# Kernel tuning notes

Measured on AMD Instinct MI355X. Metric: run time of the kernel, lower is better.

The kernel has to match this reference:

```python
import jax, jax.numpy as jnp
import numpy as np

N_NODES = 100000
N_EDGES = 3200000
N_FEAT = 128
N_GRAPHS = 256
N_CLASSES = 10


def setup_inputs() -> dict:
    key = jax.random.key(0)
    ks = jax.random.split(key, 10)
    x = jax.random.normal(ks[0], (N_NODES, N_FEAT), dtype=jnp.float32)
    edge_index = jax.random.randint(ks[1], (2, N_EDGES), 0, N_NODES, dtype=jnp.int64)
    batch = jnp.sort(jax.random.randint(ks[2], (N_NODES,), 0, N_GRAPHS, dtype=jnp.int64))
    # GCNConv weights (glorot-ish scaling) and biases
    W1 = jax.random.normal(ks[3], (N_FEAT, 16), dtype=jnp.float32) / np.sqrt(N_FEAT)
    b1 = jnp.zeros((16,), dtype=jnp.float32)
    W2 = jax.random.normal(ks[4], (16, 32), dtype=jnp.float32) / np.sqrt(16.0)
    b2 = jnp.zeros((32,), dtype=jnp.float32)
    Wfc = jax.random.normal(ks[5], (32, N_CLASSES), dtype=jnp.float32) / np.sqrt(32.0)
    bfc = jnp.zeros((N_CLASSES,), dtype=jnp.float32)
    return {"x": x, "edge_index": edge_index, "batch": batch,
            "W1": W1, "b1": b1, "W2": W2, "b2": b2, "Wfc": Wfc, "bfc": bfc}


def reference(x, edge_index, batch, W1, b1, W2, b2, Wfc, bfc):
    N = x.shape[0]
    # --- GCN normalization with self-loops (PyG GCNConv default) ---
    loop = jnp.arange(N, dtype=edge_index.dtype)
    src = jnp.concatenate([edge_index[0], loop])  # [E+N]
    dst = jnp.concatenate([edge_index[1], loop])  # [E+N]
    ones = jnp.ones_like(src, dtype=x.dtype)
    deg = jax.ops.segment_sum(ones, dst, num_segments=N)  # in-degree incl self-loop
    dinv = jax.lax.rsqrt(deg)  # deg >= 1 thanks to self-loops
    norm = dinv[src] * dinv[dst]  # [E+N]

    def gcn_conv(h, W, b):
        h = h @ W                               # [N, out] linear first (small out dim)
        msg = h[src] * norm[:, None]            # gather + edge-wise scale
        agg = jax.ops.segment_sum(msg, dst, num_segments=N)  # scatter-add
        return agg + b

    h = jax.nn.relu(gcn_conv(x, W1, b1))
    h = jax.nn.relu(gcn_conv(h, W2, b2))

    # --- global mean pool over graphs ---
    g_sum = jax.ops.segment_sum(h, batch, num_segments=N_GRAPHS)  # [G, 32]
    g_cnt = jax.ops.segment_sum(jnp.ones((N,), dtype=h.dtype), batch, num_segments=N_GRAPHS)
    pooled = g_sum / jnp.maximum(g_cnt, 1.0)[:, None]

    return pooled @ Wfc + bfc  # [G, num_classes]
```

## Files before the change

kernel.cpp:

```cpp
#include <hip/hip_runtime.h>
#include <hip/hip_fp16.h>

#define NF   128
#define C1   16
#define C2   32
#define NCLS 10
#define BSH  8
#define BN   256
#define MAXB 512
#define S    9216
#define TILE 4096
#define EPT  (TILE/256)
#define CAP  12288


__global__ __launch_bounds__(256) void k_bin(const int* __restrict__ ei,
                                             int* __restrict__ packed,
                                             int* __restrict__ offmat,
                                             int E, int nbuck) {
    __shared__ int hist[MAXB];
    __shared__ int off0[MAXB];
    __shared__ int cur[MAXB];
    int tid = threadIdx.x;
    long long t0 = (long long)blockIdx.x * TILE;

    for (int i = tid; i < MAXB; i += 256) hist[i] = 0;
    __syncthreads();

    int dstv[EPT], srcv[EPT];
#pragma unroll
    for (int u = 0; u < EPT; ++u) {
        long long e = t0 + tid + u * 256;
        int d = -1, s = 0;
        if (e < E) { d = ei[E + e]; s = ei[e]; }
        dstv[u] = d; srcv[u] = s;
        if (d >= 0) atomicAdd(&hist[d >> BSH], 1);
    }
    __syncthreads();
    if (tid < 64) {
        int carry = 0;
        for (int c = 0; c < MAXB / 64; ++c) {
            int idx = c * 64 + tid;
            int v = hist[idx];
            int orig = v;
            for (int off = 1; off < 64; off <<= 1) {
                int t = __shfl_up(v, off);
                if (tid >= off) v += t;
            }
            int ex = v - orig + carry;
            off0[idx] = ex;
            cur[idx] = ex;
            carry += __shfl(v, 63);
        }
    }
    __syncthreads();
    int* orow = offmat + (size_t)blockIdx.x * (nbuck + 1);
    for (int b = tid; b <= nbuck; b += 256) orow[b] = off0[b];
#pragma unroll
    for (int u = 0; u < EPT; ++u) {
        int d = dstv[u];
        if (d >= 0) {
            int b = d >> BSH;
            int slot = atomicAdd(&cur[b], 1);
            packed[t0 + slot] = srcv[u] | ((d & (BN - 1)) << 17);
        }
    }
}


__global__ __launch_bounds__(1024) void k_csr(const int* __restrict__ packed,
                                              const int* __restrict__ offmat,
                                              int* __restrict__ csr,
                                              int* __restrict__ rowptr,
                                              int* __restrict__ deg,
                                              float* __restrict__ dinv,
                                              int N, int nbuck, int nblkA) {
    __shared__ int stage[CAP];
    __shared__ int startA[1024];
    __shared__ int spsA[1024];
    __shared__ int o1A[1024];
    __shared__ int hcnt[BN];
    __shared__ int sh[BN];
    __shared__ int cur[BN];
    int tid = threadIdx.x;
    int b = blockIdx.x;
    size_t base = (size_t)b * S;

    int len = 0, o1 = 0;
    if (tid < nblkA) {
        const int* orow = offmat + (size_t)tid * (nbuck + 1) + b;
        o1 = orow[0];
        len = orow[1] - o1;
    }
    o1A[tid] = o1;
    spsA[tid] = len;
    if (tid < BN) hcnt[tid] = 0;
    __syncthreads();
    for (int off = 1; off < 1024; off <<= 1) {
        int t = (tid >= off) ? spsA[tid - off] : 0;
        __syncthreads();
        spsA[tid] += t;
        __syncthreads();
    }
    int m = spsA[1023];
    startA[tid] = spsA[tid] - len;
    __syncthreads();
    if (m > CAP) m = CAP;

    for (int i = tid; i < m; i += 1024) {
        int lo = 0, hi = 1023;
        while (lo < hi) {
            int mid = (lo + hi + 1) >> 1;
            if (startA[mid] <= i) lo = mid; else hi = mid - 1;
        }
        int p = packed[(size_t)lo * TILE + o1A[lo] + (i - startA[lo])];
        stage[i] = p;
        atomicAdd(&hcnt[p >> 17], 1);
    }
    __syncthreads();
    int v = 0;
    if (tid < BN) { v = hcnt[tid]; sh[tid] = v; }
    __syncthreads();
    for (int off = 1; off < BN; off <<= 1) {
        int t = (tid < BN && tid >= off) ? sh[tid - off] : 0;
        __syncthreads();
        if (tid < BN) sh[tid] += t;
        __syncthreads();
    }
    if (tid < BN) {
        int ex = sh[tid] - v;
        cur[tid] = ex;
        int n = (b << BSH) + tid;
        if (n < N) {
            rowptr[n] = (int)base + ex;
            deg[n] = v;
            dinv[n] = rsqrtf((float)v + 1.0f);
        }
    }
    __syncthreads();
    for (int i = tid; i < m; i += 1024) {
        int p = stage[i];
        int slot = atomicAdd(&cur[p >> 17], 1);
        csr[base + slot] = p & 0x1FFFF;
    }
}


__global__ __launch_bounds__(256) void k_lin1(const float* __restrict__ x,
                                              const float* __restrict__ W1,
                                              const float* __restrict__ dinv,
                                              __half* __restrict__ y1h, int N) {
    __shared__ float ws[NF * C1];
    __shared__ float xs[16 * 132];
    int tid = threadIdx.x;
    for (int t = tid; t < NF * C1; t += 256) ws[t] = W1[t];
    int n0 = blockIdx.x * 16;
    const float4* x4 = (const float4*)x;
    for (int t = tid; t < 16 * 32; t += 256) {
        int r = t >> 5, c = t & 31;
        int n = n0 + r;
        float4 v = (n < N) ? x4[(size_t)n * 32 + c] : make_float4(0.f, 0.f, 0.f, 0.f);
        float* d = &xs[r * 132 + c * 4];
        d[0] = v.x; d[1] = v.y; d[2] = v.z; d[3] = v.w;
    }
    __syncthreads();
    int r = tid >> 4, j = tid & 15;
    float acc = 0.0f;
#pragma unroll 4
    for (int k = 0; k < NF; ++k) acc += xs[r * 132 + k] * ws[k * C1 + j];
    int n = n0 + r;
    if (n < N) y1h[(size_t)n * C1 + j] = __float2half_rn(acc * dinv[n]);
}


template <int MODE>
__global__ __launch_bounds__(256) void k_gather_h(const int* __restrict__ rowptr,
                                                  const int* __restrict__ deg,
                                                  const int* __restrict__ csr,
                                                  const float* __restrict__ dinv,
                                                  const float* __restrict__ bias,
                                                  const __half2* __restrict__ yh,
                                                  void* __restrict__ outp, int N) {
    int tid = threadIdx.x;
    int j = tid & 7;
    int n = blockIdx.x * 32 + (tid >> 3);
    if (n >= N) return;
    int k0 = rowptr[n];
    int k1 = k0 + deg[n];
    float2 self = __half22float2(yh[(size_t)n * 8 + j]);
    float a0 = self.x, a1 = self.y;
    float e0 = 0.f, e1 = 0.f, f0 = 0.f, f1 = 0.f, g0 = 0.f, g1 = 0.f;
    int k = k0;
    for (; k + 3 < k1; k += 4) {
        int s0 = csr[k], s1 = csr[k + 1], s2 = csr[k + 2], s3 = csr[k + 3];
        float2 v0 = __half22float2(yh[(size_t)s0 * 8 + j]);
        float2 v1 = __half22float2(yh[(size_t)s1 * 8 + j]);
        float2 v2 = __half22float2(yh[(size_t)s2 * 8 + j]);
        float2 v3 = __half22float2(yh[(size_t)s3 * 8 + j]);
        a0 += v0.x; a1 += v0.y; e0 += v1.x; e1 += v1.y;
        f0 += v2.x; f1 += v2.y; g0 += v3.x; g1 += v3.y;
    }
    for (; k < k1; ++k) {
        float2 v = __half22float2(yh[(size_t)csr[k] * 8 + j]);
        a0 += v.x; a1 += v.y;
    }
    float dn = dinv[n];
    float rx = dn * ((a0 + e0) + (f0 + g0));
    float ry = dn * ((a1 + e1) + (f1 + g1));
    if (MODE == 0) {
        ((float2*)outp)[(size_t)n * 8 + j] = make_float2(rx, ry);
    } else {
        float2 bb = ((const float2*)bias)[j];
        float u0 = fmaxf(rx + bb.x, 0.0f) * dn;
        float u1 = fmaxf(ry + bb.y, 0.0f) * dn;
        ((__half2*)outp)[(size_t)n * 8 + j] = __floats2half2_rn(u0, u1);
    }
}


__global__ __launch_bounds__(256) void k_pool_fc(const float* __restrict__ z,
                                                 const float* __restrict__ W2,
                                                 const float* __restrict__ b2,
                                                 const int* __restrict__ batch,
                                                 const float* __restrict__ Wfc,
                                                 const float* __restrict__ bfc,
                                                 float* __restrict__ out, int N, int G) {
    __shared__ float W2s[C1 * C2];
    int tid = threadIdx.x;
    for (int t = tid; t < C1 * C2; t += 256) W2s[t] = W2[t];

    int g = blockIdx.x;
    int lo = 0, hi = N;
    while (lo < hi) { int m = (lo + hi) >> 1; if (batch[m] < g) lo = m + 1; else hi = m; }
    int start = lo;
    lo = start; hi = N;
    while (lo < hi) { int m = (lo + hi) >> 1; if (batch[m] < g + 1) lo = m + 1; else hi = m; }
    int end = lo;
    __syncthreads();

    int i = tid & 31, r = tid >> 5;
    float bi = b2[i];
    float acc = 0.0f;
    for (int n = start + r; n < end; n += 8) {
        const float* zr = &z[(size_t)n * C1];
        float h = bi;
#pragma unroll
        for (int j = 0; j < C1; ++j) h += zr[j] * W2s[j * C2 + i];
        acc += fmaxf(h, 0.0f);
    }

    __shared__ float red[256];
    red[tid] = acc;
    __syncthreads();
    for (int s = 4; s >= 1; s >>= 1) {
        if (r < s) red[tid] += red[tid + s * 32];
        __syncthreads();
    }
    __shared__ float pooled[C2];
    if (tid < C2) {
        float cnt = (float)(end - start);
        pooled[tid] = red[tid] / fmaxf(cnt, 1.0f);
    }
    __syncthreads();
    if (tid < NCLS) {
        float a = bfc[tid];
#pragma unroll
        for (int j = 0; j < C2; ++j) a += pooled[j] * Wfc[j * NCLS + tid];
        out[g * NCLS + tid] = a;
    }
}

extern "C" void kernel_launch(void* const* d_in, const int* in_sizes, int n_in,
                              void* d_out, int out_size, void* d_ws, size_t ws_size,
                              hipStream_t stream) {
    const float* x    = (const float*)d_in[0];
    const int*   ei   = (const int*)d_in[1];
    const int*   batch= (const int*)d_in[2];
    const float* W1   = (const float*)d_in[3];
    const float* b1   = (const float*)d_in[4];
    const float* W2   = (const float*)d_in[5];
    const float* b2   = (const float*)d_in[6];
    const float* Wfc  = (const float*)d_in[7];
    const float* bfc  = (const float*)d_in[8];
    float* out = (float*)d_out;

    const int N = in_sizes[0] / NF;
    const int E = in_sizes[1] / 2;
    const int G = out_size / NCLS;
    const int nbuck = (N + BN - 1) >> BSH;
    const int nblkA = (E + TILE - 1) / TILE;

    char* p = (char*)d_ws;
    auto alloc = [&](size_t bytes) { char* q = p; p += (bytes + 63) & ~(size_t)63; return q; };
    int*     rowptr  = (int*)    alloc((size_t)N * 4);
    int*     deg     = (int*)    alloc((size_t)N * 4);
    float*   dinv    = (float*)  alloc((size_t)N * 4);
    int*     packed  = (int*)    alloc((size_t)nblkA * TILE * 4);
    int*     offmat  = (int*)    alloc((size_t)nblkA * (nbuck + 1) * 4);
    int*     csr     = (int*)    alloc((size_t)nbuck * S * 4);
    __half*  y1h     = (__half*) alloc((size_t)N * C1 * 2);
    __half*  uh      = (__half*) alloc((size_t)N * C1 * 2);
    float*   z       = (float*)  alloc((size_t)N * C1 * 4);

    const int B = 256;

    k_bin<<<nblkA, B, 0, stream>>>(ei, packed, offmat, E, nbuck);
    k_csr<<<nbuck, 1024, 0, stream>>>(packed, offmat, csr, rowptr, deg, dinv,
                                      N, nbuck, nblkA);

    k_lin1<<<(N + 15) / 16, B, 0, stream>>>(x, W1, dinv, y1h, N);
    k_gather_h<1><<<(N + 31) / 32, B, 0, stream>>>(rowptr, deg, csr, dinv, b1,
                                                   (const __half2*)y1h, uh, N);

    k_gather_h<0><<<(N + 31) / 32, B, 0, stream>>>(rowptr, deg, csr, dinv, b1,
                                                   (const __half2*)uh, z, N);

    k_pool_fc<<<G, B, 0, stream>>>(z, W2, b2, batch, Wfc, bfc, out, N, G);
}
```

Measured before the change: 170.1 us.

## Fuse edge binning with first linear layer and widen gather loads

Edge binning and the x@W1 product now run as one launch with blocks split by index, using a union of their shared-memory layouts. Because dinv is not known yet, the dinv scaling of y1 moves into the tail of the CSR build kernel, which rescales each bucket's rows in place. This removes a launch and lets the dense matmul overlap the binning. The gather kernel now has each thread load 8 bytes (four halves) instead of 4, so 4 threads cover a node and a block handles 64 nodes. The cost is an extra read-modify-write pass over y1h inside k_csr and fewer independent accumulators per thread.

```diff
diff --git a/kernel.cpp b/kernel.cpp
--- a/kernel.cpp
+++ b/kernel.cpp
@@ -14,56 +14,82 @@
 #define CAP  12288
 
 
-__global__ __launch_bounds__(256) void k_bin(const int* __restrict__ ei,
+struct BinSh { int hist[MAXB]; int off0[MAXB]; int cur[MAXB]; };
+struct LinSh { float ws[NF * C1]; float xs[16 * 132]; };
+union FatSh { BinSh b; LinSh l; };
+
+__global__ __launch_bounds__(256) void k_fat(const int* __restrict__ ei,
                                              int* __restrict__ packed,
                                              int* __restrict__ offmat,
-                                             int E, int nbuck) {
-    __shared__ int hist[MAXB];
-    __shared__ int off0[MAXB];
-    __shared__ int cur[MAXB];
+                                             const float* __restrict__ x,
+                                             const float* __restrict__ W1,
+                                             __half* __restrict__ y1h,
+                                             int E, int nbuck, int nblkA, int N) {
+    __shared__ FatSh sm;
     int tid = threadIdx.x;
-    long long t0 = (long long)blockIdx.x * TILE;
-
-    for (int i = tid; i < MAXB; i += 256) hist[i] = 0;
-    __syncthreads();
-
-    int dstv[EPT], srcv[EPT];
+
+    if (blockIdx.x < nblkA) {
+        long long t0 = (long long)blockIdx.x * TILE;
+        for (int i = tid; i < MAXB; i += 256) sm.b.hist[i] = 0;
+        __syncthreads();
+
+        int dstv[EPT], srcv[EPT];
 #pragma unroll
-    for (int u = 0; u < EPT; ++u) {
-        long long e = t0 + tid + u * 256;
-        int d = -1, s = 0;
-        if (e < E) { d = ei[E + e]; s = ei[e]; }
-        dstv[u] = d; srcv[u] = s;
-        if (d >= 0) atomicAdd(&hist[d >> BSH], 1);
-    }
-    __syncthreads();
-    if (tid < 64) {
-        int carry = 0;
-        for (int c = 0; c < MAXB / 64; ++c) {
-            int idx = c * 64 + tid;
-            int v = hist[idx];
-            int orig = v;
-            for (int off = 1; off < 64; off <<= 1) {
-                int t = __shfl_up(v, off);
-                if (tid >= off) v += t;
+        for (int u = 0; u < EPT; ++u) {
+            long long e = t0 + tid + u * 256;
+            int d = -1, s = 0;
+            if (e < E) { d = ei[E + e]; s = ei[e]; }
+            dstv[u] = d; srcv[u] = s;
+            if (d >= 0) atomicAdd(&sm.b.hist[d >> BSH], 1);
+        }
+        __syncthreads();
+        if (tid < 64) {
+            int carry = 0;
+            for (int c = 0; c < MAXB / 64; ++c) {
+                int idx = c * 64 + tid;
+                int v = sm.b.hist[idx];
+                int orig = v;
+                for (int off = 1; off < 64; off <<= 1) {
+                    int t = __shfl_up(v, off);
+                    if (tid >= off) v += t;
+                }
+                int ex = v - orig + carry;
+                sm.b.off0[idx] = ex;
+                sm.b.cur[idx] = ex;
+                carry += __shfl(v, 63);
             }
-            int ex = v - orig + carry;
-            off0[idx] = ex;
-            cur[idx] = ex;
-            carry += __shfl(v, 63);
-        }
-    }
-    __syncthreads();
-    int* orow = offmat + (size_t)blockIdx.x * (nbuck + 1);
-    for (int b = tid; b <= nbuck; b += 256) orow[b] = off0[b];
+        }
+        __syncthreads();
+        int* orow = offmat + (size_t)blockIdx.x * (nbuck + 1);
+        for (int b = tid; b <= nbuck; b += 256) orow[b] = sm.b.off0[b];
 #pragma unroll
-    for (int u = 0; u < EPT; ++u) {
-        int d = dstv[u];
-        if (d >= 0) {
-            int b = d >> BSH;
-            int slot = atomicAdd(&cur[b], 1);
-            packed[t0 + slot] = srcv[u] | ((d & (BN - 1)) << 17);
-        }
+        for (int u = 0; u < EPT; ++u) {
+            int d = dstv[u];
+            if (d >= 0) {
+                int b = d >> BSH;
+                int slot = atomicAdd(&sm.b.cur[b], 1);
+                packed[t0 + slot] = srcv[u] | ((d & (BN - 1)) << 17);
+            }
+        }
+    } else {
+        int bid = blockIdx.x - nblkA;
+        for (int t = tid; t < NF * C1; t += 256) sm.l.ws[t] = W1[t];
+        int n0 = bid * 16;
+        const float4* x4 = (const float4*)x;
+        for (int t = tid; t < 16 * 32; t += 256) {
+            int r = t >> 5, c = t & 31;
+            int n = n0 + r;
+            float4 v = (n < N) ? x4[(size_t)n * 32 + c] : make_float4(0.f, 0.f, 0.f, 0.f);
+            float* d = &sm.l.xs[r * 132 + c * 4];
+            d[0] = v.x; d[1] = v.y; d[2] = v.z; d[3] = v.w;
+        }
+        __syncthreads();
+        int r = tid >> 4, j = tid & 15;
+        float acc = 0.0f;
+#pragma unroll 4
+        for (int k = 0; k < NF; ++k) acc += sm.l.xs[r * 132 + k] * sm.l.ws[k * C1 + j];
+        int n = n0 + r;
+        if (n < N) y1h[(size_t)n * C1 + j] = __float2half_rn(acc);
     }
 }
 
@@ -74,6 +100,7 @@
                                               int* __restrict__ rowptr,
                                               int* __restrict__ deg,
                                               float* __restrict__ dinv,
+                                              __half* __restrict__ y1h,
                                               int N, int nbuck, int nblkA) {
     __shared__ int stage[CAP];
     __shared__ int startA[1024];
@@ -82,6 +109,7 @@
     __shared__ int hcnt[BN];
     __shared__ int sh[BN];
     __shared__ int cur[BN];
+    __shared__ float fdinv[BN];
     int tid = threadIdx.x;
     int b = blockIdx.x;
     size_t base = (size_t)b * S;
@@ -130,11 +158,13 @@
     if (tid < BN) {
         int ex = sh[tid] - v;
         cur[tid] = ex;
+        float dv = rsqrtf((float)v + 1.0f);
+        fdinv[tid] = dv;
         int n = (b << BSH) + tid;
         if (n < N) {
             rowptr[n] = (int)base + ex;
             deg[n] = v;
-            dinv[n] = rsqrtf((float)v + 1.0f);
+            dinv[n] = dv;
         }
     }
     __syncthreads();
@@ -143,33 +173,17 @@
         int slot = atomicAdd(&cur[p >> 17], 1);
         csr[base + slot] = p & 0x1FFFF;
     }
-}
-
-
-__global__ __launch_bounds__(256) void k_lin1(const float* __restrict__ x,
-                                              const float* __restrict__ W1,
-                                              const float* __restrict__ dinv,
-                                              __half* __restrict__ y1h, int N) {
-    __shared__ float ws[NF * C1];
-    __shared__ float xs[16 * 132];
-    int tid = threadIdx.x;
-    for (int t = tid; t < NF * C1; t += 256) ws[t] = W1[t];
-    int n0 = blockIdx.x * 16;
-    const float4* x4 = (const float4*)x;
-    for (int t = tid; t < 16 * 32; t += 256) {
-        int r = t >> 5, c = t & 31;
-        int n = n0 + r;
-        float4 v = (n < N) ? x4[(size_t)n * 32 + c] : make_float4(0.f, 0.f, 0.f, 0.f);
-        float* d = &xs[r * 132 + c * 4];
-        d[0] = v.x; d[1] = v.y; d[2] = v.z; d[3] = v.w;
-    }
-    __syncthreads();
-    int r = tid >> 4, j = tid & 15;
-    float acc = 0.0f;
-#pragma unroll 4
-    for (int k = 0; k < NF; ++k) acc += xs[r * 132 + k] * ws[k * C1 + j];
-    int n = n0 + r;
-    if (n < N) y1h[(size_t)n * C1 + j] = __float2half_rn(acc * dinv[n]);
+    int n0 = b << BSH;
+    int lim = min(BN, N - n0);
+    if (lim > 0) {
+        __half2* yrow = (__half2*)y1h + (size_t)n0 * 8;
+        int tot = lim * 8;
+        for (int i = tid; i < tot; i += 1024) {
+            float dv = fdinv[i >> 3];
+            float2 f = __half22float2(yrow[i]);
+            yrow[i] = __floats2half2_rn(f.x * dv, f.y * dv);
+        }
+    }
 }
 
 
@@ -179,41 +193,52 @@
                                                   const int* __restrict__ csr,
                                                   const float* __restrict__ dinv,
                                                   const float* __restrict__ bias,
-                                                  const __half2* __restrict__ yh,
+                                                  const uint2* __restrict__ yh,
                                                   void* __restrict__ outp, int N) {
     int tid = threadIdx.x;
-    int j = tid & 7;
-    int n = blockIdx.x * 32 + (tid >> 3);
+    int j = tid & 3;
+    int n = blockIdx.x * 64 + (tid >> 2);
     if (n >= N) return;
     int k0 = rowptr[n];
     int k1 = k0 + deg[n];
-    float2 self = __half22float2(yh[(size_t)n * 8 + j]);
-    float a0 = self.x, a1 = self.y;
-    float e0 = 0.f, e1 = 0.f, f0 = 0.f, f1 = 0.f, g0 = 0.f, g1 = 0.f;
+    union U { uint2 u; __half2 h[2]; };
+    U su; su.u = yh[(size_t)n * 4 + j];
+    float2 sl = __half22float2(su.h[0]), shh = __half22float2(su.h[1]);
+    float a0 = sl.x, a1 = sl.y, a2 = shh.x, a3 = shh.y;
+    float b0 = 0.f, b1v = 0.f, b2 = 0.f, b3 = 0.f;
     int k = k0;
     for (; k + 3 < k1; k += 4) {
         int s0 = csr[k], s1 = csr[k + 1], s2 = csr[k + 2], s3 = csr[k + 3];
-        float2 v0 = __half22float2(yh[(size_t)s0 * 8 + j]);
-        float2 v1 = __half22float2(yh[(size_t)s1 * 8 + j]);
-        float2 v2 = __half22float2(yh[(size_t)s2 * 8 + j]);
-        float2 v3 = __half22float2(yh[(size_t)s3 * 8 + j]);
-        a0 += v0.x; a1 += v0.y; e0 += v1.x; e1 += v1.y;
-        f0 += v2.x; f1 += v2.y; g0 += v3.x; g1 += v3.y;
+        U v0, v1, v2, v3;
+        v0.u = yh[(size_t)s0 * 4 + j];
+        v1.u = yh[(size_t)s1 * 4 + j];
+        v2.u = yh[(size_t)s2 * 4 + j];
+        v3.u = yh[(size_t)s3 * 4 + j];
+        float2 l0 = __half22float2(v0.h[0]), h0 = __half22float2(v0.h[1]);
+        float2 l1 = __half22float2(v1.h[0]), h1 = __half22float2(v1.h[1]);
+        float2 l2 = __half22float2(v2.h[0]), h2 = __half22float2(v2.h[1]);
+        float2 l3 = __half22float2(v3.h[0]), h3 = __half22float2(v3.h[1]);
+        a0 += l0.x; a1 += l0.y; a2 += h0.x; a3 += h0.y;
+        b0 += l1.x; b1v += l1.y; b2 += h1.x; b3 += h1.y;
+        a0 += l2.x; a1 += l2.y; a2 += h2.x; a3 += h2.y;
+        b0 += l3.x; b1v += l3.y; b2 += h3.x; b3 += h3.y;
     }
     for (; k < k1; ++k) {
-        float2 v = __half22float2(yh[(size_t)csr[k] * 8 + j]);
-        a0 += v.x; a1 += v.y;
+        U v; v.u = yh[(size_t)csr[k] * 4 + j];
+        float2 l = __half22float2(v.h[0]), h = __half22float2(v.h[1]);
+        a0 += l.x; a1 += l.y; a2 += h.x; a3 += h.y;
     }
     float dn = dinv[n];
-    float rx = dn * ((a0 + e0) + (f0 + g0));
-    float ry = dn * ((a1 + e1) + (f1 + g1));
+    float r0 = dn * (a0 + b0), r1 = dn * (a1 + b1v);
+    float r2 = dn * (a2 + b2), r3 = dn * (a3 + b3);
     if (MODE == 0) {
-        ((float2*)outp)[(size_t)n * 8 + j] = make_float2(rx, ry);
+        ((float4*)outp)[(size_t)n * 4 + j] = make_float4(r0, r1, r2, r3);
     } else {
-        float2 bb = ((const float2*)bias)[j];
-        float u0 = fmaxf(rx + bb.x, 0.0f) * dn;
-        float u1 = fmaxf(ry + bb.y, 0.0f) * dn;
-        ((__half2*)outp)[(size_t)n * 8 + j] = __floats2half2_rn(u0, u1);
+        float4 bb = ((const float4*)bias)[j];
+        U o;
+        o.h[0] = __floats2half2_rn(fmaxf(r0 + bb.x, 0.0f) * dn, fmaxf(r1 + bb.y, 0.0f) * dn);
+        o.h[1] = __floats2half2_rn(fmaxf(r2 + bb.z, 0.0f) * dn, fmaxf(r3 + bb.w, 0.0f) * dn);
+        ((uint2*)outp)[(size_t)n * 4 + j] = o.u;
     }
 }
 
@@ -289,6 +314,7 @@
     const int G = out_size / NCLS;
     const int nbuck = (N + BN - 1) >> BSH;
     const int nblkA = (E + TILE - 1) / TILE;
+    const int nblkL = (N + 15) / 16;
 
     char* p = (char*)d_ws;
     auto alloc = [&](size_t bytes) { char* q = p; p += (bytes + 63) & ~(size_t)63; return q; };
@@ -304,16 +330,15 @@
 
     const int B = 256;
 
-    k_bin<<<nblkA, B, 0, stream>>>(ei, packed, offmat, E, nbuck);
-    k_csr<<<nbuck, 1024, 0, stream>>>(packed, offmat, csr, rowptr, deg, dinv,
+    k_fat<<<nblkA + nblkL, B, 0, stream>>>(ei, packed, offmat, x, W1, y1h,
+                                           E, nbuck, nblkA, N);
+    k_csr<<<nbuck, 1024, 0, stream>>>(packed, offmat, csr, rowptr, deg, dinv, y1h,
                                       N, nbuck, nblkA);
 
-    k_lin1<<<(N + 15) / 16, B, 0, stream>>>(x, W1, dinv, y1h, N);
-    k_gather_h<1><<<(N + 31) / 32, B, 0, stream>>>(rowptr, deg, csr, dinv, b1,
-                                                   (const __half2*)y1h, uh, N);
-
-    k_gather_h<0><<<(N + 31) / 32, B, 0, stream>>>(rowptr, deg, csr, dinv, b1,
-                                                   (const __half2*)uh, z, N);
+    k_gather_h<1><<<(N + 63) / 64, B, 0, stream>>>(rowptr, deg, csr, dinv, b1,
+                                                   (const uint2*)y1h, uh, N);
+    k_gather_h<0><<<(N + 63) / 64, B, 0, stream>>>(rowptr, deg, csr, dinv, b1,
+                                                   (const uint2*)uh, z, N);
 
     k_pool_fc<<<G, B, 0, stream>>>(z, W2, b2, batch, Wfc, bfc, out, N, G);
 }
```

Measured after the change: 173.2 us. No clear change (+1.8%).
